# Performance work log

Hardware: AMD Instinct MI355X
Metric: run time of the kernel (lower is better)

Reference implementation:

```python
import jax, jax.numpy as jnp
import numpy as np

B, T, D = 4, 1024, 1024
N_HEAD, HEAD, LATENT = 16, 64, 32
N_EXP, TOP_K, N_FF = 8, 2, 4096
HID = int(2 * N_FF / 3)  # 2730, Expert hidden when ffn_multiplier is None
CAP_FACTOR = 1.0


def setup_inputs() -> dict:
    key = jax.random.key(0)
    ks = jax.random.split(key, 14)
    s = 0.02
    f = lambda k, shp: jax.random.normal(k, shp, jnp.float32) * s
    return dict(
        x=jax.random.normal(ks[0], (B, T, D), jnp.float32),
        noise_eps=jax.random.normal(ks[1], (B, T, N_EXP), jnp.float32),
        ln1_w=jnp.ones((D,), jnp.float32),
        ln2_w=jnp.ones((D,), jnp.float32),
        q_w=f(ks[2], (N_HEAD, D, HEAD)), q_b=jnp.zeros((N_HEAD, HEAD), jnp.float32),
        ka_w=f(ks[3], (N_HEAD, D, LATENT)), kb_w=f(ks[4], (N_HEAD, LATENT, HEAD)),
        va_w=f(ks[5], (N_HEAD, D, LATENT)), vb_w=f(ks[6], (N_HEAD, LATENT, HEAD)),
        proj_w=f(ks[7], (D, D)), proj_b=jnp.zeros((D,), jnp.float32),
        route_w=f(ks[8], (D, N_EXP)), route_b=jnp.zeros((N_EXP,), jnp.float32),
        noise_w=f(ks[9], (D, N_EXP)), noise_b=jnp.zeros((N_EXP,), jnp.float32),
        swiglu_w=f(ks[10], (N_EXP, D, 2 * HID)),
        down_w=f(ks[11], (N_EXP, HID, D)),
    )


def _rms(x, w, eps=1e-5):
    x32 = x.astype(jnp.float32)
    n = x32 * jax.lax.rsqrt(jnp.mean(x32 * x32, -1, keepdims=True) + eps)
    return n.astype(x.dtype) * w


def _rope(q, k):
    # q,k: [B,H,T,hd]; even/odd split then concatenated halves (matches torch code)
    hd, Tq = q.shape[-1], q.shape[-2]
    inv = 1.0 / (10000.0 ** (jnp.arange(0, hd, 2, dtype=jnp.float32) / hd))
    ang = jnp.arange(Tq, dtype=jnp.float32)[:, None] * inv[None, :]  # [T, hd/2]
    cos, sin = jnp.cos(ang), jnp.sin(ang)
    def rot(t):
        t1, t2 = t[..., ::2], t[..., 1::2]
        return jnp.concatenate([t1 * cos - t2 * sin, t1 * sin + t2 * cos], -1)
    return rot(q), rot(k)


def reference(x, noise_eps, ln1_w, ln2_w, q_w, q_b, ka_w, kb_w, va_w, vb_w,
              proj_w, proj_b, route_w, route_b, noise_w, noise_b, swiglu_w, down_w):
    Bx, Tx, Dm = x.shape
    hd = q_w.shape[-1]
    E = route_w.shape[-1]
    # ---- Multi-Head Latent Attention (pre-norm) ----
    xn = _rms(x, ln1_w)
    q = jnp.einsum('btd,hde->bhte', xn, q_w) + q_b[None, :, None, :]
    k = jnp.einsum('bhtl,hle->bhte', jnp.einsum('btd,hdl->bhtl', xn, ka_w), kb_w)
    v = jnp.einsum('bhtl,hle->bhte', jnp.einsum('btd,hdl->bhtl', xn, va_w), vb_w)
    q, k = _rope(q, k)
    scores = jnp.einsum('bhtd,bhsd->bhts', q, k) / jnp.sqrt(jnp.float32(hd))
    attn = jax.nn.softmax(scores, axis=-1)  # NOTE: no causal mask in source
    o = jnp.einsum('bhts,bhsd->bhtd', attn, v)
    o = o.transpose(0, 2, 1, 3).reshape(Bx, Tx, Dm)
    x = x + (o @ proj_w + proj_b)
    # ---- Noisy top-k router ----
    xn2 = _rms(x, ln2_w)
    logits = xn2 @ route_w + route_b
    noisy = logits + noise_eps * jax.nn.softplus(xn2 @ noise_w + noise_b)  # temperature=1
    _, topi = jax.lax.top_k(noisy, TOP_K)  # [B,T,k]
    sel = jnp.any(jax.nn.one_hot(topi, E, dtype=jnp.bool_), axis=-2)  # [B,T,E]
    probs = jax.nn.softmax(jnp.where(sel, noisy, -jnp.inf), axis=-1)
    aux = jnp.sum((jnp.mean(probs, (0, 1)) - 1.0 / E) ** 2)
    # ---- Capacity-limited expert dispatch (first-come in flat token order) ----
    N = Bx * Tx
    cap = int(N * TOP_K / E * CAP_FACTOR)
    flat_x = xn2.reshape(N, Dm)
    flat_p = probs.reshape(N, E)
    flat_i = topi.reshape(N, TOP_K)
    upd = jnp.zeros((N, Dm), x.dtype)
    for e in range(E):
        m = jnp.any(flat_i == e, axis=-1)            # [N]
        pos = jnp.cumsum(m) - 1                      # slot within expert buffer
        keep = m & (pos < cap)
        slot = jnp.where(keep, pos, cap)             # dropped -> overflow slot
        tok = jnp.zeros(cap + 1, jnp.int32).at[slot].set(jnp.arange(N, dtype=jnp.int32))[:cap]
        valid = jnp.zeros(cap + 1, jnp.bool_).at[slot].set(keep)[:cap]
        xe = flat_x[tok] * valid[:, None]            # [cap, D]; zero rows yield zero output (no biases)
        h = xe @ swiglu_w[e]
        h1, h2 = jnp.split(h, 2, axis=-1)
        oe = (jax.nn.silu(h1) * h2) @ down_w[e]
        gate = jnp.where(valid, flat_p[tok, e], 0.0)
        upd = upd.at[tok].add(oe * gate[:, None])
    return x + upd.reshape(Bx, Tx, Dm), aux
```

## Files before the change

### kernel.cpp

```cpp
#include <hip/hip_runtime.h>
#include <math.h>

#define NTOK   4096
#define DM     1024
#define NHEAD  16
#define HDIM   64
#define NEXP   8
#define CAP    1024
#define HID    2730
#define NFF2   5460
#define HIDP   2752

typedef __attribute__((ext_vector_type(8))) short bf16x8;
typedef __attribute__((ext_vector_type(4))) float f32x4;
typedef __attribute__((ext_vector_type(8))) _Float16 h16x8;
typedef __attribute__((ext_vector_type(4))) _Float16 h16x4;
typedef __attribute__((ext_vector_type(8))) unsigned short u16x8;

__device__ __forceinline__ unsigned short f2bf(float f) {
  unsigned int u = __float_as_uint(f);
  u += 0x7fffu + ((u >> 16) & 1u);
  return (unsigned short)(u >> 16);
}

__global__ void pack_kernel(const float* __restrict__ q_w, const float* __restrict__ ka_w,
                            const float* __restrict__ va_w, float* __restrict__ Wq,
                            float* __restrict__ Wlat) {
  int idx = blockIdx.x * 256 + threadIdx.x;
  if (idx < 1048576) {
    int d = idx >> 10, nn = idx & 1023;
    int h = nn >> 6, e = nn & 63;
    Wq[idx] = q_w[((size_t)h * 1024 + d) * 64 + e];
  } else {
    int j = idx - 1048576;
    int d = j >> 10, nn = j & 1023;
    if (nn < 512) {
      int h = nn >> 5, l = nn & 31;
      Wlat[j] = ka_w[((size_t)h * 1024 + d) * 32 + l];
    } else {
      int c = nn - 512;
      int h = c >> 5, l = c & 31;
      Wlat[j] = va_w[((size_t)h * 1024 + d) * 32 + l];
    }
  }
}

__global__ __launch_bounds__(256) void pack_swiglu(const float* __restrict__ swiglu_w,
                                                   unsigned short* __restrict__ Wpk) {
  int b = blockIdx.x;
  int kc32 = b & 31;
  int ejt = b >> 5;
  int jt = ejt % 43;
  int e = ejt / 43;
  int tid = threadIdx.x;
  int col = tid & 63;
  int k0 = (tid >> 6) * 8;
  int n = jt * 64 + col;
  bool nv = n < HID;
  const float* src = swiglu_w + ((size_t)e * DM + kc32 * 32 + k0) * NFF2 + n;
  u16x8 o1, o2;
#pragma unroll
  for (int j = 0; j < 8; j++) {
    float v1 = nv ? src[(size_t)j * NFF2] : 0.f;
    float v2 = nv ? src[(size_t)j * NFF2 + HID] : 0.f;
    o1[j] = f2bf(v1);
    o2[j] = f2bf(v2);
  }
  unsigned short* dst = Wpk + (size_t)b * 4096 + col * 32 + k0;
  *(u16x8*)dst = o1;
  *(u16x8*)(dst + 2048) = o2;
}

template <bool DUAL>
__global__ __launch_bounds__(256) void rms_kernel(const float* __restrict__ x,
                                                  const float* __restrict__ w,
                                                  float* __restrict__ out,
                                                  unsigned short* __restrict__ outb) {
  int row = blockIdx.x;
  int tid = threadIdx.x;
  const float4 v = ((const float4*)(x + (size_t)row * DM))[tid];
  float ss = v.x * v.x + v.y * v.y + v.z * v.z + v.w * v.w;
#pragma unroll
  for (int off = 32; off >= 1; off >>= 1) ss += __shfl_down(ss, off);
  __shared__ float red[4];
  if ((tid & 63) == 0) red[tid >> 6] = ss;
  __syncthreads();
  float tot = red[0] + red[1] + red[2] + red[3];
  float scale = rsqrtf(tot * (1.0f / 1024.0f) + 1e-5f);
  const float4 wv = ((const float4*)w)[tid];
  float4 o;
  o.x = v.x * scale * wv.x; o.y = v.y * scale * wv.y;
  o.z = v.z * scale * wv.z; o.w = v.w * scale * wv.w;
  ((float4*)(out + (size_t)row * DM))[tid] = o;
  if (DUAL) {
    ushort4 ob;
    ob.x = f2bf(o.x); ob.y = f2bf(o.y); ob.z = f2bf(o.z); ob.w = f2bf(o.w);
    *(ushort4*)(outb + (size_t)row * DM + tid * 4) = ob;
  }
}

template <bool BIAS, bool RES>
__global__ __launch_bounds__(256) void mfma_dense(const float* __restrict__ A,
                                                  const float* __restrict__ Bm,
                                                  const float* __restrict__ bias,
                                                  const float* __restrict__ res,
                                                  float* __restrict__ C, int K, int N) {
  int m0 = blockIdx.x * 128;
  int n0 = blockIdx.y * 128;
  __shared__ short As[128][40];
  __shared__ short Bs[128][40];
  int tid = threadIdx.x;
  int wid = tid >> 6, lane = tid & 63;
  int wm0 = (wid >> 1) * 64, wn0 = (wid & 1) * 64;
  int lr = lane & 15, lq = lane >> 4;
  f32x4 c[4][4];
  f32x4 zz = {0.f, 0.f, 0.f, 0.f};
#pragma unroll
  for (int i = 0; i < 4; i++)
#pragma unroll
    for (int j = 0; j < 4; j++) c[i][j] = zz;
  int ar = tid >> 2;
  int aq = tid & 3;
  int bn = tid & 127;
  int bh = tid >> 7;
  const float* Bp = Bm + n0 + bn;
  for (int kc = 0; kc < K; kc += 32) {
    __syncthreads();
#pragma unroll
    for (int rr = 0; rr < 2; rr++) {
      int row = rr * 64 + ar;
      const float* ap = A + (size_t)(m0 + row) * K + kc + aq * 8;
      float4 a0 = *(const float4*)ap;
      float4 a1 = *(const float4*)(ap + 4);
      u16x8 pk;
      pk[0] = f2bf(a0.x); pk[1] = f2bf(a0.y); pk[2] = f2bf(a0.z); pk[3] = f2bf(a0.w);
      pk[4] = f2bf(a1.x); pk[5] = f2bf(a1.y); pk[6] = f2bf(a1.z); pk[7] = f2bf(a1.w);
      *(u16x8*)&As[row][aq * 8] = pk;
    }
    {
      const float* bp = Bp + (size_t)(kc + bh * 16) * N;
      u16x8 p0, p1;
#pragma unroll
      for (int j = 0; j < 8; j++) p0[j] = f2bf(bp[(size_t)j * N]);
#pragma unroll
      for (int j = 0; j < 8; j++) p1[j] = f2bf(bp[(size_t)(j + 8) * N]);
      *(u16x8*)&Bs[bn][bh * 16] = p0;
      *(u16x8*)&Bs[bn][bh * 16 + 8] = p1;
    }
    __syncthreads();
    bf16x8 a[4], b[4];
#pragma unroll
    for (int mi = 0; mi < 4; mi++) a[mi] = *(bf16x8*)&As[wm0 + mi * 16 + lr][lq * 8];
#pragma unroll
    for (int ni = 0; ni < 4; ni++) b[ni] = *(bf16x8*)&Bs[wn0 + ni * 16 + lr][lq * 8];
#pragma unroll
    for (int mi = 0; mi < 4; mi++)
#pragma unroll
      for (int ni = 0; ni < 4; ni++)
        c[mi][ni] = __builtin_amdgcn_mfma_f32_16x16x32_bf16(a[mi], b[ni], c[mi][ni], 0, 0, 0);
  }
#pragma unroll
  for (int mi = 0; mi < 4; mi++)
#pragma unroll
    for (int ni = 0; ni < 4; ni++) {
      int nn = n0 + wn0 + ni * 16 + lr;
      float bv = BIAS ? bias[nn] : 0.f;
#pragma unroll
      for (int r = 0; r < 4; r++) {
        int mm = m0 + wm0 + mi * 16 + lq * 4 + r;
        float v = c[mi][ni][r] + bv;
        if (RES) v += res[(size_t)mm * N + nn];
        C[(size_t)mm * N + nn] = v;
      }
    }
}

__global__ void expand_kernel(const float* __restrict__ latents, const float* __restrict__ kb_w,
                              const float* __restrict__ vb_w, float* __restrict__ kpre,
                              _Float16* __restrict__ vf) {
  int idx = blockIdx.x * 256 + threadIdx.x;
  int e = idx & 63;
  int t = (idx >> 6) & 1023;
  int h = (idx >> 16) & 15;
  int b = idx >> 20;
  const float* lrow = latents + ((size_t)(b * 1024 + t)) * DM;
  const float* kb = kb_w + (size_t)h * 2048;
  const float* vb = vb_w + (size_t)h * 2048;
  float ka = 0.f, va = 0.f;
#pragma unroll
  for (int l = 0; l < 32; l++) {
    ka += lrow[h * 32 + l] * kb[l * 64 + e];
    va += lrow[512 + h * 32 + l] * vb[l * 64 + e];
  }
  kpre[idx] = ka;
  vf[idx] = (_Float16)va;
}

template <bool IN_BTHD>
__global__ void rope_kernel(const float* __restrict__ in, _Float16* __restrict__ out) {
  int idx = blockIdx.x * 256 + threadIdx.x;
  int i = idx & 31;
  int t = (idx >> 5) & 1023;
  int h = (idx >> 15) & 15;
  int b = idx >> 19;
  size_t ib;
  if (IN_BTHD)
    ib = ((size_t)(b * 1024 + t)) * DM + h * 64;
  else
    ib = ((size_t)((b * 16 + h) * 1024 + t)) * 64;
  float t1 = in[ib + 2 * i], t2 = in[ib + 2 * i + 1];
  float inv = exp2f(-(float)i * 0.41524101186091903f);
  float ang = (float)t * inv;
  float s, c;
  sincosf(ang, &s, &c);
  size_t ob = ((size_t)((b * 16 + h) * 1024 + t)) * 64;
  out[ob + i] = (_Float16)(t1 * c - t2 * s);
  out[ob + 32 + i] = (_Float16)(t1 * s + t2 * c);
}

__global__ __launch_bounds__(256) void attn_mfma(const _Float16* __restrict__ qf,
                                                 const _Float16* __restrict__ kf,
                                                 const _Float16* __restrict__ vf,
                                                 float* __restrict__ o) {
  __shared__ _Float16 Ks[64][72];
  __shared__ _Float16 Vt[64][68];
  int bh = blockIdx.y;
  int q0 = blockIdx.x * 64;
  int tid = threadIdx.x;
  int wv = tid >> 6, lane = tid & 63;
  int lr = lane & 15, lq = lane >> 4;
  const size_t base = (size_t)bh * 1024 * 64;
  const _Float16* qrow = qf + base + (size_t)(q0 + wv * 16 + lr) * 64;
  h16x8 qfr[2];
  qfr[0] = *(const h16x8*)(qrow + lq * 8);
  qfr[1] = *(const h16x8*)(qrow + 32 + lq * 8);
  float mrow = -3.0e38f, lsum = 0.f;
  f32x4 oacc[4];
  f32x4 zz = {0.f, 0.f, 0.f, 0.f};
#pragma unroll
  for (int i = 0; i < 4; i++) oacc[i] = zz;
  int skey = tid >> 2, spart = tid & 3;
  int vkey = tid & 63, vdb = (tid >> 6) * 16;

  for (int kt = 0; kt < 16; kt++) {
    __syncthreads();
    {
      const _Float16* kg = kf + base + (size_t)(kt * 64 + skey) * 64 + spart * 16;
      *(h16x8*)&Ks[skey][spart * 16] = *(const h16x8*)kg;
      *(h16x8*)&Ks[skey][spart * 16 + 8] = *(const h16x8*)(kg + 8);
      const _Float16* vg = vf + base + (size_t)(kt * 64 + vkey) * 64 + vdb;
      h16x8 v0 = *(const h16x8*)vg;
      h16x8 v1 = *(const h16x8*)(vg + 8);
#pragma unroll
      for (int j = 0; j < 8; j++) {
        Vt[vdb + j][vkey] = v0[j];
        Vt[vdb + 8 + j][vkey] = v1[j];
      }
    }
    __syncthreads();
    f32x4 st[4];
#pragma unroll
    for (int ni = 0; ni < 4; ni++) {
      st[ni] = zz;
#pragma unroll
      for (int kc = 0; kc < 2; kc++) {
        h16x8 ak = *(const h16x8*)&Ks[ni * 16 + lr][kc * 32 + lq * 8];
        st[ni] = __builtin_amdgcn_mfma_f32_16x16x32_f16(ak, qfr[kc], st[ni], 0, 0, 0);
      }
    }
    float smax = -3.0e38f;
#pragma unroll
    for (int ni = 0; ni < 4; ni++)
#pragma unroll
      for (int r = 0; r < 4; r++) {
        st[ni][r] *= 0.125f;
        smax = fmaxf(smax, st[ni][r]);
      }
    smax = fmaxf(smax, __shfl_xor(smax, 16));
    smax = fmaxf(smax, __shfl_xor(smax, 32));
    float newm = fmaxf(mrow, smax);
    float alpha = expf(mrow - newm);
    float rsum = 0.f;
    h16x4 pf[4];
#pragma unroll
    for (int ni = 0; ni < 4; ni++)
#pragma unroll
      for (int r = 0; r < 4; r++) {
        float p = expf(st[ni][r] - newm);
        rsum += p;
        pf[ni][r] = (_Float16)p;
      }
    rsum += __shfl_xor(rsum, 16);
    rsum += __shfl_xor(rsum, 32);
    lsum = lsum * alpha + rsum;
    mrow = newm;
#pragma unroll
    for (int dt = 0; dt < 4; dt++) {
      oacc[dt][0] *= alpha; oacc[dt][1] *= alpha;
      oacc[dt][2] *= alpha; oacc[dt][3] *= alpha;
    }
#pragma unroll
    for (int dt = 0; dt < 4; dt++)
#pragma unroll
      for (int ni = 0; ni < 4; ni++) {
        h16x4 va = *(const h16x4*)&Vt[dt * 16 + lr][ni * 16 + lq * 4];
        oacc[dt] = __builtin_amdgcn_mfma_f32_16x16x16f16(va, pf[ni], oacc[dt], 0, 0, 0);
      }
  }
  int b = bh >> 4, h = bh & 15;
  int qg = q0 + wv * 16 + lr;
  float invl = 1.0f / lsum;
  float* orow = o + (size_t)(b * 1024 + qg) * DM + h * 64;
#pragma unroll
  for (int dt = 0; dt < 4; dt++)
#pragma unroll
    for (int r = 0; r < 4; r++) orow[dt * 16 + lq * 4 + r] = oacc[dt][r] * invl;
}

__global__ __launch_bounds__(256) void router_kernel(
    const float* __restrict__ xn2, const float* __restrict__ route_w,
    const float* __restrict__ route_b, const float* __restrict__ noise_w,
    const float* __restrict__ noise_b, const float* __restrict__ noise_eps,
    int* __restrict__ topi, float* __restrict__ flat_p, float* __restrict__ probsum,
    int* __restrict__ slotmap) {
  int wave = threadIdx.x >> 6;
  int lane = threadIdx.x & 63;
  int tk = blockIdx.x * 4 + wave;
  float acc[8] = {0.f}, nacc[8] = {0.f};
  const float* xr = xn2 + (size_t)tk * DM;
  for (int it = 0; it < 16; it++) {
    int d = it * 64 + lane;
    float xv = xr[d];
    const float* rw = route_w + d * 8;
    const float* nw = noise_w + d * 8;
#pragma unroll
    for (int e = 0; e < 8; e++) {
      acc[e] += xv * rw[e];
      nacc[e] += xv * nw[e];
    }
  }
#pragma unroll
  for (int off = 32; off >= 1; off >>= 1) {
#pragma unroll
    for (int e = 0; e < 8; e++) {
      acc[e] += __shfl_down(acc[e], off);
      nacc[e] += __shfl_down(nacc[e], off);
    }
  }
  if (lane == 0) {
    float noisy[8];
#pragma unroll
    for (int e = 0; e < 8; e++) {
      float lg = acc[e] + route_b[e];
      float nl = nacc[e] + noise_b[e];
      float sp = (nl > 20.f) ? nl : log1pf(expf(nl));
      noisy[e] = lg + noise_eps[tk * 8 + e] * sp;
    }
    int i1 = 0;
    float n1 = noisy[0];
#pragma unroll
    for (int e = 1; e < 8; e++)
      if (noisy[e] > n1) { n1 = noisy[e]; i1 = e; }
    int i2 = -1;
    float n2 = -3.0e38f;
#pragma unroll
    for (int e = 0; e < 8; e++)
      if (e != i1 && noisy[e] > n2) { n2 = noisy[e]; i2 = e; }
    float r = expf(n2 - n1);
    float p1 = 1.0f / (1.0f + r);
    float p2 = r / (1.0f + r);
    topi[tk * 2] = i1;
    topi[tk * 2 + 1] = i2;
#pragma unroll
    for (int e = 0; e < 8; e++) flat_p[tk * 8 + e] = (e == i1) ? p1 : ((e == i2) ? p2 : 0.f);
    atomicAdd(&probsum[i1], p1);
    atomicAdd(&probsum[i2], p2);
    slotmap[tk * 2] = -1;
    slotmap[tk * 2 + 1] = -1;
  }
}

__global__ __launch_bounds__(512) void scan_kernel(const int* __restrict__ topi,
                                                   const float* __restrict__ flat_p,
                                                   int* __restrict__ tok, float* __restrict__ gate,
                                                   int* __restrict__ cnt, int* __restrict__ slotmap) {
  int e = threadIdx.x >> 6;
  int lane = threadIdx.x & 63;
  int count = 0;
  for (int base = 0; base < NTOK; base += 64) {
    int t = base + lane;
    int a = topi[t * 2], b = topi[t * 2 + 1];
    bool mflag = (a == e) || (b == e);
    unsigned long long mask = __ballot(mflag);
    int pos = count + __popcll(mask & ((1ull << lane) - 1ull));
    if (mflag && pos < CAP) {
      tok[e * CAP + pos] = t;
      gate[e * CAP + pos] = flat_p[t * 8 + e];
      int k = (a == e) ? 0 : 1;
      slotmap[t * 2 + k] = pos;
    }
    count += __popcll(mask);
  }
  if (lane == 0) cnt[e] = (count < CAP) ? count : CAP;
}

template <bool PACKED>
__global__ __launch_bounds__(256) void mfma_swiglu(const unsigned short* __restrict__ xn2b,
                                                   const float* __restrict__ swiglu_w,
                                                   const unsigned short* __restrict__ Wpk,
                                                   const int* __restrict__ tok,
                                                   const int* __restrict__ cnt,
                                                   unsigned short* __restrict__ ACT) {
  int L = blockIdx.x;
  int e = L & 7;
  int gw = L >> 3;
  int m0 = (gw & 7) * 128;
  int jt = gw >> 3;
  int j0 = jt * 64;
  __shared__ short As[128][40];
  __shared__ short B1s[64][40];
  __shared__ short B2s[64][40];
  __shared__ int tokL[128];
  int tid = threadIdx.x;
  if (tid < 128) {
    int slot = m0 + tid;
    tokL[tid] = (slot < cnt[e]) ? tok[e * CAP + slot] : -1;
  }
  __syncthreads();
  int wid = tid >> 6, lane = tid & 63;
  int wm0 = (wid >> 1) * 64, wn0 = (wid & 1) * 32;
  int lr = lane & 15, lq = lane >> 4;
  f32x4 c1[4][2], c2[4][2];
  f32x4 zz = {0.f, 0.f, 0.f, 0.f};
#pragma unroll
  for (int i = 0; i < 4; i++)
#pragma unroll
    for (int j = 0; j < 2; j++) { c1[i][j] = zz; c2[i][j] = zz; }
  int ar = tid >> 2;
  int aq = tid & 3;
  int tr0 = tokL[ar], tr1 = tokL[64 + ar];
  const unsigned short* wbase = Wpk + (size_t)(e * 43 + jt) * 32 * 4096;
  int bnn = tid & 63;
  int bkq = tid >> 6;
  int col = j0 + bnn;
  bool cvalid = col < HID;
  const float* Wb = swiglu_w + (size_t)e * DM * NFF2;
  const float* Wc1 = Wb + col;
  const float* Wc2 = Wb + HID + col;

  for (int kc = 0; kc < DM; kc += 32) {
    __syncthreads();
    {
      float4 av = {0.f, 0.f, 0.f, 0.f};
      if (tr0 >= 0) av = *(const float4*)(xn2b + (size_t)tr0 * DM + kc + aq * 8);
      *(float4*)&As[ar][aq * 8] = av;
      float4 av2 = {0.f, 0.f, 0.f, 0.f};
      if (tr1 >= 0) av2 = *(const float4*)(xn2b + (size_t)tr1 * DM + kc + aq * 8);
      *(float4*)&As[64 + ar][aq * 8] = av2;
    }
    if (PACKED) {
      const unsigned short* wp = wbase + (size_t)(kc >> 5) * 4096;
      u16x8 k1 = *(const u16x8*)(wp + tid * 8);
      u16x8 k2 = *(const u16x8*)(wp + 2048 + tid * 8);
      *(u16x8*)&B1s[tid >> 2][(tid & 3) * 8] = k1;
      *(u16x8*)&B2s[tid >> 2][(tid & 3) * 8] = k2;
    } else {
      const float* p1 = Wc1 + (size_t)(kc + bkq * 8) * NFF2;
      const float* p2 = Wc2 + (size_t)(kc + bkq * 8) * NFF2;
      u16x8 k1, k2;
#pragma unroll
      for (int j = 0; j < 8; j++) {
        float v1 = cvalid ? p1[(size_t)j * NFF2] : 0.f;
        float v2 = cvalid ? p2[(size_t)j * NFF2] : 0.f;
        k1[j] = f2bf(v1);
        k2[j] = f2bf(v2);
      }
      *(u16x8*)&B1s[bnn][bkq * 8] = k1;
      *(u16x8*)&B2s[bnn][bkq * 8] = k2;
    }
    __syncthreads();
    bf16x8 a[4], b1[2], b2[2];
#pragma unroll
    for (int mi = 0; mi < 4; mi++) a[mi] = *(bf16x8*)&As[wm0 + mi * 16 + lr][lq * 8];
#pragma unroll
    for (int ni = 0; ni < 2; ni++) {
      b1[ni] = *(bf16x8*)&B1s[wn0 + ni * 16 + lr][lq * 8];
      b2[ni] = *(bf16x8*)&B2s[wn0 + ni * 16 + lr][lq * 8];
    }
#pragma unroll
    for (int mi = 0; mi < 4; mi++)
#pragma unroll
      for (int ni = 0; ni < 2; ni++) {
        c1[mi][ni] = __builtin_amdgcn_mfma_f32_16x16x32_bf16(a[mi], b1[ni], c1[mi][ni], 0, 0, 0);
        c2[mi][ni] = __builtin_amdgcn_mfma_f32_16x16x32_bf16(a[mi], b2[ni], c2[mi][ni], 0, 0, 0);
      }
  }
#pragma unroll
  for (int mi = 0; mi < 4; mi++)
#pragma unroll
    for (int ni = 0; ni < 2; ni++)
#pragma unroll
      for (int r = 0; r < 4; r++) {
        int mm = m0 + wm0 + mi * 16 + lq * 4 + r;
        int cc = j0 + wn0 + ni * 16 + lr;
        float h1 = c1[mi][ni][r], h2 = c2[mi][ni][r];
        float act = (h1 / (1.0f + expf(-h1))) * h2;
        ACT[(size_t)e * CAP * HIDP + (size_t)mm * HIDP + cc] = f2bf(act);
      }
}

__global__ __launch_bounds__(256) void mfma_down(const unsigned short* __restrict__ ACT,
                                                 const float* __restrict__ down_w,
                                                 float* __restrict__ OE) {
  int L = blockIdx.x;
  int e = L & 7;
  int gw = L >> 3;
  int m0 = (gw & 7) * 128;
  int n0 = (gw >> 3) * 128;
  __shared__ short As[128][40];
  __shared__ short Bs[128][40];
  int tid = threadIdx.x;
  int wid = tid >> 6, lane = tid & 63;
  int wm0 = (wid >> 1) * 64, wn0 = (wid & 1) * 64;
  int lr = lane & 15, lq = lane >> 4;
  f32x4 c[4][4];
  f32x4 zz = {0.f, 0.f, 0.f, 0.f};
#pragma unroll
  for (int i = 0; i < 4; i++)
#pragma unroll
    for (int j = 0; j < 4; j++) c[i][j] = zz;
  const unsigned short* Ab = ACT + (size_t)e * CAP * HIDP + (size_t)m0 * HIDP;
  const float* Bb = down_w + (size_t)e * HID * DM + n0;
  int ar = tid >> 2;
  int aq = tid & 3;
  int bnn = tid & 127;
  int bh = tid >> 7;
  const float* Bp = Bb + bnn;

  for (int kc = 0; kc < HIDP; kc += 32) {
    __syncthreads();
    *(float4*)&As[ar][aq * 8] = *(const float4*)(Ab + (size_t)ar * HIDP + kc + aq * 8);
    *(float4*)&As[64 + ar][aq * 8] = *(const float4*)(Ab + (size_t)(64 + ar) * HIDP + kc + aq * 8);
    {
      int kb = kc + bh * 16;
      u16x8 p0, p1;
#pragma unroll
      for (int j = 0; j < 8; j++) {
        float v = (kb + j < HID) ? Bp[(size_t)(kb + j) * DM] : 0.f;
        p0[j] = f2bf(v);
      }
#pragma unroll
      for (int j = 0; j < 8; j++) {
        float v = (kb + 8 + j < HID) ? Bp[(size_t)(kb + 8 + j) * DM] : 0.f;
        p1[j] = f2bf(v);
      }
      *(u16x8*)&Bs[bnn][bh * 16] = p0;
      *(u16x8*)&Bs[bnn][bh * 16 + 8] = p1;
    }
    __syncthreads();
    bf16x8 a[4], b[4];
#pragma unroll
    for (int mi = 0; mi < 4; mi++) a[mi] = *(bf16x8*)&As[wm0 + mi * 16 + lr][lq * 8];
#pragma unroll
    for (int ni = 0; ni < 4; ni++) b[ni] = *(bf16x8*)&Bs[wn0 + ni * 16 + lr][lq * 8];
#pragma unroll
    for (int mi = 0; mi < 4; mi++)
#pragma unroll
      for (int ni = 0; ni < 4; ni++)
        c[mi][ni] = __builtin_amdgcn_mfma_f32_16x16x32_bf16(a[mi], b[ni], c[mi][ni], 0, 0, 0);
  }
#pragma unroll
  for (int mi = 0; mi < 4; mi++)
#pragma unroll
    for (int ni = 0; ni < 4; ni++)
#pragma unroll
      for (int r = 0; r < 4; r++) {
        int mm = m0 + wm0 + mi * 16 + lq * 4 + r;
        int nn = n0 + wn0 + ni * 16 + lr;
        OE[((size_t)e << 20) + (size_t)mm * DM + nn] = c[mi][ni][r];
      }
}

__global__ void combine_kernel(const float* __restrict__ x2, const float* __restrict__ OE,
                               const int* __restrict__ topi, const int* __restrict__ slotmap,
                               const float* __restrict__ flat_p, float* __restrict__ out) {
  int idx = blockIdx.x * 256 + threadIdx.x;
  int t = idx >> 8;
  int c4 = (idx & 255) * 4;
  float4 v = *(const float4*)(x2 + (size_t)t * DM + c4);
#pragma unroll
  for (int k = 0; k < 2; k++) {
    int s = slotmap[t * 2 + k];
    if (s >= 0) {
      int e = topi[t * 2 + k];
      float g = flat_p[t * 8 + e];
      float4 ov = *(const float4*)(OE + ((size_t)e << 20) + (size_t)s * DM + c4);
      v.x += g * ov.x; v.y += g * ov.y; v.z += g * ov.z; v.w += g * ov.w;
    }
  }
  *(float4*)(out + (size_t)t * DM + c4) = v;
}

__global__ void aux_kernel(const float* __restrict__ probsum, float* __restrict__ out) {
  if (threadIdx.x == 0) {
    float s = 0.f;
#pragma unroll
    for (int e = 0; e < 8; e++) {
      float d = probsum[e] * (1.0f / 4096.0f) - 0.125f;
      s += d * d;
    }
    out[4194304] = s;
  }
}

extern "C" void kernel_launch(void* const* d_in, const int* in_sizes, int n_in, void* d_out,
                              int out_size, void* d_ws, size_t ws_size, hipStream_t stream) {
  const float* x = (const float*)d_in[0];
  const float* noise_eps = (const float*)d_in[1];
  const float* ln1_w = (const float*)d_in[2];
  const float* ln2_w = (const float*)d_in[3];
  const float* q_w = (const float*)d_in[4];
  const float* q_b = (const float*)d_in[5];
  const float* ka_w = (const float*)d_in[6];
  const float* kb_w = (const float*)d_in[7];
  const float* va_w = (const float*)d_in[8];
  const float* vb_w = (const float*)d_in[9];
  const float* proj_w = (const float*)d_in[10];
  const float* proj_b = (const float*)d_in[11];
  const float* route_w = (const float*)d_in[12];
  const float* route_b = (const float*)d_in[13];
  const float* noise_w = (const float*)d_in[14];
  const float* noise_b = (const float*)d_in[15];
  const float* swiglu_w = (const float*)d_in[16];
  const float* down_w = (const float*)d_in[17];
  float* out = (float*)d_out;
  char* w = (char*)d_ws;
  const size_t MB = 1ull << 20;

  bool packed = ws_size >= (size_t)172 * MB;

  float* xn = (float*)(w + 0 * MB);
  float* qtmp = (float*)(w + 16 * MB);
  float* latents = (float*)(w + 32 * MB);
  float* kpre = (float*)(w + 48 * MB);
  _Float16* qfb = (_Float16*)(w + 64 * MB);
  _Float16* kfb = (_Float16*)(w + 72 * MB);
  _Float16* vfb = (_Float16*)(w + 80 * MB);
  float* ob = (float*)(w + 88 * MB);
  float* Wq = (float*)(w + 104 * MB);
  float* Wlat = (float*)(w + 108 * MB);
  float* x2 = (float*)(w + 44 * MB);
  float* xn2 = (float*)(w + 60 * MB);
  unsigned short* Wpk = (unsigned short*)(w + 76 * MB);
  unsigned short* ACT = (unsigned short*)(w + 0 * MB);
  float* OE = (float*)(w + 76 * MB);
  unsigned short* xn2b = (unsigned short*)(w + (packed ? 162 : 108) * MB);
  char* sm = w + (packed ? 170 : 116) * MB;
  int* topi = (int*)sm;
  int* tok = (int*)(sm + 64 * 1024);
  int* cntb = (int*)(sm + 128 * 1024);
  int* slotmap = (int*)(sm + 192 * 1024);
  float* flat_p = (float*)(sm + 256 * 1024);
  float* gateb = (float*)(sm + 512 * 1024);
  float* probsum = (float*)(sm + 576 * 1024);

  pack_kernel<<<8192, 256, 0, stream>>>(q_w, ka_w, va_w, Wq, Wlat);
  rms_kernel<false><<<4096, 256, 0, stream>>>(x, ln1_w, xn, nullptr);
  mfma_dense<true, false><<<dim3(32, 8), 256, 0, stream>>>(xn, Wq, q_b, nullptr, qtmp, 1024, 1024);
  mfma_dense<false, false><<<dim3(32, 8), 256, 0, stream>>>(xn, Wlat, nullptr, nullptr, latents, 1024, 1024);
  expand_kernel<<<16384, 256, 0, stream>>>(latents, kb_w, vb_w, kpre, vfb);
  rope_kernel<true><<<8192, 256, 0, stream>>>(qtmp, qfb);
  rope_kernel<false><<<8192, 256, 0, stream>>>(kpre, kfb);
  attn_mfma<<<dim3(16, 64), 256, 0, stream>>>(qfb, kfb, vfb, ob);
  mfma_dense<true, true><<<dim3(32, 8), 256, 0, stream>>>(ob, proj_w, proj_b, x, x2, 1024, 1024);
  if (packed) {
    pack_swiglu<<<11008, 256, 0, stream>>>(swiglu_w, Wpk);
  }
  rms_kernel<true><<<4096, 256, 0, stream>>>(x2, ln2_w, xn2, xn2b);
  hipMemsetAsync(probsum, 0, 8 * sizeof(float), stream);
  router_kernel<<<1024, 256, 0, stream>>>(xn2, route_w, route_b, noise_w, noise_b, noise_eps,
                                          topi, flat_p, probsum, slotmap);
  scan_kernel<<<1, 512, 0, stream>>>(topi, flat_p, tok, gateb, cntb, slotmap);
  if (packed) {
    mfma_swiglu<true><<<2752, 256, 0, stream>>>(xn2b, swiglu_w, Wpk, tok, cntb, ACT);
  } else {
    mfma_swiglu<false><<<2752, 256, 0, stream>>>(xn2b, swiglu_w, Wpk, tok, cntb, ACT);
  }
  mfma_down<<<512, 256, 0, stream>>>(ACT, down_w, OE);
  combine_kernel<<<4096, 256, 0, stream>>>(x2, OE, topi, slotmap, flat_p, out);
  aux_kernel<<<1, 64, 0, stream>>>(probsum, out);
}
```

Measured before the change: 1.086 ms.

## Pre-pack all GEMM weights to bf16 tiles and prefetch operands in registers

Adds packing kernels that convert the q/latent/proj and down-projection weights into bf16 k-tiled layouts, so the GEMM inner loops do coalesced vector loads instead of strided fp32 loads with per-element conversion. Activations feeding the dense GEMMs (RMS output, attention output) are now stored as bf16. All MFMA GEMMs gain a register prefetch of the next k-tile that overlaps global loads with compute. The workspace layout is reorganised and the unpacked fallback path is removed. In exchange, extra pack passes over down_w and proj_w are added every call, and the workspace must be large enough for the packed buffers.

```diff
diff --git a/kernel.cpp b/kernel.cpp
--- a/kernel.cpp
+++ b/kernel.cpp
@@ -10,6 +10,7 @@
 #define HID    2730
 #define NFF2   5460
 #define HIDP   2752
+#define KCD    86
 
 typedef __attribute__((ext_vector_type(8))) short bf16x8;
 typedef __attribute__((ext_vector_type(4))) float f32x4;
@@ -23,25 +24,43 @@
   return (unsigned short)(u >> 16);
 }
 
-__global__ void pack_kernel(const float* __restrict__ q_w, const float* __restrict__ ka_w,
-                            const float* __restrict__ va_w, float* __restrict__ Wq,
-                            float* __restrict__ Wlat) {
-  int idx = blockIdx.x * 256 + threadIdx.x;
-  if (idx < 1048576) {
-    int d = idx >> 10, nn = idx & 1023;
-    int h = nn >> 6, e = nn & 63;
-    Wq[idx] = q_w[((size_t)h * 1024 + d) * 64 + e];
+__global__ __launch_bounds__(256) void pack_dense3(const float* __restrict__ q_w,
+                                                   const float* __restrict__ ka_w,
+                                                   const float* __restrict__ va_w,
+                                                   const float* __restrict__ proj_w,
+                                                   unsigned short* __restrict__ Wqt,
+                                                   unsigned short* __restrict__ Wlatt,
+                                                   unsigned short* __restrict__ Wprojt) {
+  int b = blockIdx.x;
+  int tid = threadIdx.x;
+  int col = tid & 63;
+  int k0 = (tid >> 6) * 8;
+  int which = b >> 9;
+  int bb = b & 511;
+  int nt = bb >> 5, kc = bb & 31;
+  int d0 = kc * 32 + k0;
+  u16x8 o;
+  if (which == 0) {
+    const float* src = q_w + ((size_t)nt * 1024 + d0) * 64 + col;
+#pragma unroll
+    for (int j = 0; j < 8; j++) o[j] = f2bf(src[(size_t)j * 64]);
+    *(u16x8*)(Wqt + (size_t)bb * 2048 + col * 32 + k0) = o;
+  } else if (which == 1) {
+    int n = nt * 64 + col;
+    const float* base;
+    int h, l;
+    if (n < 512) { h = n >> 5; l = n & 31; base = ka_w; }
+    else { int m = n - 512; h = m >> 5; l = m & 31; base = va_w; }
+    const float* src = base + ((size_t)h * 1024 + d0) * 32 + l;
+#pragma unroll
+    for (int j = 0; j < 8; j++) o[j] = f2bf(src[(size_t)j * 32]);
+    *(u16x8*)(Wlatt + (size_t)bb * 2048 + col * 32 + k0) = o;
   } else {
-    int j = idx - 1048576;
-    int d = j >> 10, nn = j & 1023;
-    if (nn < 512) {
-      int h = nn >> 5, l = nn & 31;
-      Wlat[j] = ka_w[((size_t)h * 1024 + d) * 32 + l];
-    } else {
-      int c = nn - 512;
-      int h = c >> 5, l = c & 31;
-      Wlat[j] = va_w[((size_t)h * 1024 + d) * 32 + l];
-    }
+    int n = nt * 64 + col;
+    const float* src = proj_w + (size_t)d0 * 1024 + n;
+#pragma unroll
+    for (int j = 0; j < 8; j++) o[j] = f2bf(src[(size_t)j * 1024]);
+    *(u16x8*)(Wprojt + (size_t)bb * 2048 + col * 32 + k0) = o;
   }
 }
 
@@ -71,7 +90,28 @@
   *(u16x8*)(dst + 2048) = o2;
 }
 
-template <bool DUAL>
+__global__ __launch_bounds__(256) void pack_down(const float* __restrict__ down_w,
+                                                 unsigned short* __restrict__ Wdk) {
+  int b = blockIdx.x;
+  int kci = b % KCD;
+  int ent = b / KCD;
+  int nt = ent & 15;
+  int e = ent >> 4;
+  int tid = threadIdx.x;
+  int col = tid & 63, k0 = (tid >> 6) * 8;
+  int n = nt * 64 + col;
+  int kbase = kci * 32 + k0;
+  const float* src = down_w + ((size_t)e * HID + kbase) * DM + n;
+  u16x8 o;
+#pragma unroll
+  for (int j = 0; j < 8; j++) {
+    float v = (kbase + j < HID) ? src[(size_t)j * DM] : 0.f;
+    o[j] = f2bf(v);
+  }
+  *(u16x8*)(Wdk + (size_t)b * 2048 + col * 32 + k0) = o;
+}
+
+template <bool F32OUT>
 __global__ __launch_bounds__(256) void rms_kernel(const float* __restrict__ x,
                                                   const float* __restrict__ w,
                                                   float* __restrict__ out,
@@ -91,22 +131,21 @@
   float4 o;
   o.x = v.x * scale * wv.x; o.y = v.y * scale * wv.y;
   o.z = v.z * scale * wv.z; o.w = v.w * scale * wv.w;
-  ((float4*)(out + (size_t)row * DM))[tid] = o;
-  if (DUAL) {
-    ushort4 ob;
-    ob.x = f2bf(o.x); ob.y = f2bf(o.y); ob.z = f2bf(o.z); ob.w = f2bf(o.w);
-    *(ushort4*)(outb + (size_t)row * DM + tid * 4) = ob;
-  }
+  if (F32OUT) ((float4*)(out + (size_t)row * DM))[tid] = o;
+  ushort4 ob;
+  ob.x = f2bf(o.x); ob.y = f2bf(o.y); ob.z = f2bf(o.z); ob.w = f2bf(o.w);
+  *(ushort4*)(outb + (size_t)row * DM + tid * 4) = ob;
 }
 
 template <bool BIAS, bool RES>
-__global__ __launch_bounds__(256) void mfma_dense(const float* __restrict__ A,
-                                                  const float* __restrict__ Bm,
+__global__ __launch_bounds__(256) void mfma_dense(const unsigned short* __restrict__ A,
+                                                  const unsigned short* __restrict__ Bpk,
                                                   const float* __restrict__ bias,
                                                   const float* __restrict__ res,
                                                   float* __restrict__ C, int K, int N) {
   int m0 = blockIdx.x * 128;
   int n0 = blockIdx.y * 128;
+  int KC = K >> 5;
   __shared__ short As[128][40];
   __shared__ short Bs[128][40];
   int tid = threadIdx.x;
@@ -119,35 +158,27 @@
   for (int i = 0; i < 4; i++)
 #pragma unroll
     for (int j = 0; j < 4; j++) c[i][j] = zz;
-  int ar = tid >> 2;
-  int aq = tid & 3;
-  int bn = tid & 127;
-  int bh = tid >> 7;
-  const float* Bp = Bm + n0 + bn;
-  for (int kc = 0; kc < K; kc += 32) {
-    __syncthreads();
-#pragma unroll
-    for (int rr = 0; rr < 2; rr++) {
-      int row = rr * 64 + ar;
-      const float* ap = A + (size_t)(m0 + row) * K + kc + aq * 8;
-      float4 a0 = *(const float4*)ap;
-      float4 a1 = *(const float4*)(ap + 4);
-      u16x8 pk;
-      pk[0] = f2bf(a0.x); pk[1] = f2bf(a0.y); pk[2] = f2bf(a0.z); pk[3] = f2bf(a0.w);
-      pk[4] = f2bf(a1.x); pk[5] = f2bf(a1.y); pk[6] = f2bf(a1.z); pk[7] = f2bf(a1.w);
-      *(u16x8*)&As[row][aq * 8] = pk;
-    }
-    {
-      const float* bp = Bp + (size_t)(kc + bh * 16) * N;
-      u16x8 p0, p1;
-#pragma unroll
-      for (int j = 0; j < 8; j++) p0[j] = f2bf(bp[(size_t)j * N]);
-#pragma unroll
-      for (int j = 0; j < 8; j++) p1[j] = f2bf(bp[(size_t)(j + 8) * N]);
-      *(u16x8*)&Bs[bn][bh * 16] = p0;
-      *(u16x8*)&Bs[bn][bh * 16 + 8] = p1;
-    }
-    __syncthreads();
+  int ar = tid >> 2, aq = tid & 3;
+  const unsigned short* Ap0 = A + (size_t)(m0 + ar) * K + aq * 8;
+  const unsigned short* Ap1 = A + (size_t)(m0 + 64 + ar) * K + aq * 8;
+  const unsigned short* Bt = Bpk + (size_t)(n0 >> 6) * KC * 2048 + tid * 8;
+  u16x8 ra0 = *(const u16x8*)Ap0;
+  u16x8 ra1 = *(const u16x8*)Ap1;
+  u16x8 rb0 = *(const u16x8*)Bt;
+  u16x8 rb1 = *(const u16x8*)(Bt + (size_t)KC * 2048);
+  for (int kci = 0; kci < KC; kci++) {
+    __syncthreads();
+    *(u16x8*)&As[ar][aq * 8] = ra0;
+    *(u16x8*)&As[64 + ar][aq * 8] = ra1;
+    *(u16x8*)&Bs[tid >> 2][(tid & 3) * 8] = rb0;
+    *(u16x8*)&Bs[64 + (tid >> 2)][(tid & 3) * 8] = rb1;
+    __syncthreads();
+    if (kci + 1 < KC) {
+      ra0 = *(const u16x8*)(Ap0 + (kci + 1) * 32);
+      ra1 = *(const u16x8*)(Ap1 + (kci + 1) * 32);
+      rb0 = *(const u16x8*)(Bt + (size_t)(kci + 1) * 2048);
+      rb1 = *(const u16x8*)(Bt + (size_t)(KC + kci + 1) * 2048);
+    }
     bf16x8 a[4], b[4];
 #pragma unroll
     for (int mi = 0; mi < 4; mi++) a[mi] = *(bf16x8*)&As[wm0 + mi * 16 + lr][lq * 8];
@@ -221,7 +252,7 @@
 __global__ __launch_bounds__(256) void attn_mfma(const _Float16* __restrict__ qf,
                                                  const _Float16* __restrict__ kf,
                                                  const _Float16* __restrict__ vf,
-                                                 float* __restrict__ o) {
+                                                 unsigned short* __restrict__ o) {
   __shared__ _Float16 Ks[64][72];
   __shared__ _Float16 Vt[64][68];
   int bh = blockIdx.y;
@@ -310,11 +341,16 @@
   int b = bh >> 4, h = bh & 15;
   int qg = q0 + wv * 16 + lr;
   float invl = 1.0f / lsum;
-  float* orow = o + (size_t)(b * 1024 + qg) * DM + h * 64;
-#pragma unroll
-  for (int dt = 0; dt < 4; dt++)
-#pragma unroll
-    for (int r = 0; r < 4; r++) orow[dt * 16 + lq * 4 + r] = oacc[dt][r] * invl;
+  unsigned short* orow = o + (size_t)(b * 1024 + qg) * DM + h * 64;
+#pragma unroll
+  for (int dt = 0; dt < 4; dt++) {
+    ushort4 ov;
+    ov.x = f2bf(oacc[dt][0] * invl);
+    ov.y = f2bf(oacc[dt][1] * invl);
+    ov.z = f2bf(oacc[dt][2] * invl);
+    ov.w = f2bf(oacc[dt][3] * invl);
+    *(ushort4*)(orow + dt * 16 + lq * 4) = ov;
+  }
 }
 
 __global__ __launch_bounds__(256) void router_kernel(
@@ -404,9 +440,7 @@
   if (lane == 0) cnt[e] = (count < CAP) ? count : CAP;
 }
 
-template <bool PACKED>
 __global__ __launch_bounds__(256) void mfma_swiglu(const unsigned short* __restrict__ xn2b,
-                                                   const float* __restrict__ swiglu_w,
                                                    const unsigned short* __restrict__ Wpk,
                                                    const int* __restrict__ tok,
                                                    const int* __restrict__ cnt,
@@ -424,7 +458,7 @@
   int tid = threadIdx.x;
   if (tid < 128) {
     int slot = m0 + tid;
-    tokL[tid] = (slot < cnt[e]) ? tok[e * CAP + slot] : -1;
+    tokL[tid] = (slot < cnt[e]) ? tok[e * CAP + slot] : 0;
   }
   __syncthreads();
   int wid = tid >> 6, lane = tid & 63;
@@ -436,49 +470,28 @@
   for (int i = 0; i < 4; i++)
 #pragma unroll
     for (int j = 0; j < 2; j++) { c1[i][j] = zz; c2[i][j] = zz; }
-  int ar = tid >> 2;
-  int aq = tid & 3;
-  int tr0 = tokL[ar], tr1 = tokL[64 + ar];
-  const unsigned short* wbase = Wpk + (size_t)(e * 43 + jt) * 32 * 4096;
-  int bnn = tid & 63;
-  int bkq = tid >> 6;
-  int col = j0 + bnn;
-  bool cvalid = col < HID;
-  const float* Wb = swiglu_w + (size_t)e * DM * NFF2;
-  const float* Wc1 = Wb + col;
-  const float* Wc2 = Wb + HID + col;
-
-  for (int kc = 0; kc < DM; kc += 32) {
-    __syncthreads();
-    {
-      float4 av = {0.f, 0.f, 0.f, 0.f};
-      if (tr0 >= 0) av = *(const float4*)(xn2b + (size_t)tr0 * DM + kc + aq * 8);
-      *(float4*)&As[ar][aq * 8] = av;
-      float4 av2 = {0.f, 0.f, 0.f, 0.f};
-      if (tr1 >= 0) av2 = *(const float4*)(xn2b + (size_t)tr1 * DM + kc + aq * 8);
-      *(float4*)&As[64 + ar][aq * 8] = av2;
-    }
-    if (PACKED) {
-      const unsigned short* wp = wbase + (size_t)(kc >> 5) * 4096;
-      u16x8 k1 = *(const u16x8*)(wp + tid * 8);
-      u16x8 k2 = *(const u16x8*)(wp + 2048 + tid * 8);
-      *(u16x8*)&B1s[tid >> 2][(tid & 3) * 8] = k1;
-      *(u16x8*)&B2s[tid >> 2][(tid & 3) * 8] = k2;
-    } else {
-      const float* p1 = Wc1 + (size_t)(kc + bkq * 8) * NFF2;
-      const float* p2 = Wc2 + (size_t)(kc + bkq * 8) * NFF2;
-      u16x8 k1, k2;
-#pragma unroll
-      for (int j = 0; j < 8; j++) {
-        float v1 = cvalid ? p1[(size_t)j * NFF2] : 0.f;
-        float v2 = cvalid ? p2[(size_t)j * NFF2] : 0.f;
-        k1[j] = f2bf(v1);
-        k2[j] = f2bf(v2);
-      }
-      *(u16x8*)&B1s[bnn][bkq * 8] = k1;
-      *(u16x8*)&B2s[bnn][bkq * 8] = k2;
-    }
-    __syncthreads();
+  int ar = tid >> 2, aq = tid & 3;
+  const unsigned short* Ap0 = xn2b + (size_t)tokL[ar] * DM + aq * 8;
+  const unsigned short* Ap1 = xn2b + (size_t)tokL[64 + ar] * DM + aq * 8;
+  const unsigned short* wp = Wpk + (size_t)(e * 43 + jt) * 32 * 4096 + tid * 8;
+  u16x8 ra0 = *(const u16x8*)Ap0;
+  u16x8 ra1 = *(const u16x8*)Ap1;
+  u16x8 rb1 = *(const u16x8*)wp;
+  u16x8 rb2 = *(const u16x8*)(wp + 2048);
+
+  for (int kci = 0; kci < 32; kci++) {
+    __syncthreads();
+    *(u16x8*)&As[ar][aq * 8] = ra0;
+    *(u16x8*)&As[64 + ar][aq * 8] = ra1;
+    *(u16x8*)&B1s[tid >> 2][(tid & 3) * 8] = rb1;
+    *(u16x8*)&B2s[tid >> 2][(tid & 3) * 8] = rb2;
+    __syncthreads();
+    if (kci < 31) {
+      ra0 = *(const u16x8*)(Ap0 + (kci + 1) * 32);
+      ra1 = *(const u16x8*)(Ap1 + (kci + 1) * 32);
+      rb1 = *(const u16x8*)(wp + (size_t)(kci + 1) * 4096);
+      rb2 = *(const u16x8*)(wp + (size_t)(kci + 1) * 4096 + 2048);
+    }
     bf16x8 a[4], b1[2], b2[2];
 #pragma unroll
     for (int mi = 0; mi < 4; mi++) a[mi] = *(bf16x8*)&As[wm0 + mi * 16 + lr][lq * 8];
@@ -510,13 +523,14 @@
 }
 
 __global__ __launch_bounds__(256) void mfma_down(const unsigned short* __restrict__ ACT,
-                                                 const float* __restrict__ down_w,
+                                                 const unsigned short* __restrict__ Wdk,
                                                  float* __restrict__ OE) {
   int L = blockIdx.x;
   int e = L & 7;
   int gw = L >> 3;
   int m0 = (gw & 7) * 128;
-  int n0 = (gw >> 3) * 128;
+  int nt0 = (gw >> 3) * 2;
+  int n0 = nt0 * 64;
   __shared__ short As[128][40];
   __shared__ short Bs[128][40];
   int tid = threadIdx.x;
@@ -529,35 +543,29 @@
   for (int i = 0; i < 4; i++)
 #pragma unroll
     for (int j = 0; j < 4; j++) c[i][j] = zz;
+  int ar = tid >> 2, aq = tid & 3;
   const unsigned short* Ab = ACT + (size_t)e * CAP * HIDP + (size_t)m0 * HIDP;
-  const float* Bb = down_w + (size_t)e * HID * DM + n0;
-  int ar = tid >> 2;
-  int aq = tid & 3;
-  int bnn = tid & 127;
-  int bh = tid >> 7;
-  const float* Bp = Bb + bnn;
-
-  for (int kc = 0; kc < HIDP; kc += 32) {
-    __syncthreads();
-    *(float4*)&As[ar][aq * 8] = *(const float4*)(Ab + (size_t)ar * HIDP + kc + aq * 8);
-    *(float4*)&As[64 + ar][aq * 8] = *(const float4*)(Ab + (size_t)(64 + ar) * HIDP + kc + aq * 8);
-    {
-      int kb = kc + bh * 16;
-      u16x8 p0, p1;
-#pragma unroll
-      for (int j = 0; j < 8; j++) {
-        float v = (kb + j < HID) ? Bp[(size_t)(kb + j) * DM] : 0.f;
-        p0[j] = f2bf(v);
-      }
-#pragma unroll
-      for (int j = 0; j < 8; j++) {
-        float v = (kb + 8 + j < HID) ? Bp[(size_t)(kb + 8 + j) * DM] : 0.f;
-        p1[j] = f2bf(v);
-      }
-      *(u16x8*)&Bs[bnn][bh * 16] = p0;
-      *(u16x8*)&Bs[bnn][bh * 16 + 8] = p1;
-    }
-    __syncthreads();
+  const unsigned short* Ap0 = Ab + (size_t)ar * HIDP + aq * 8;
+  const unsigned short* Ap1 = Ab + (size_t)(64 + ar) * HIDP + aq * 8;
+  const unsigned short* Bt = Wdk + (size_t)(e * 16 + nt0) * KCD * 2048 + tid * 8;
+  u16x8 ra0 = *(const u16x8*)Ap0;
+  u16x8 ra1 = *(const u16x8*)Ap1;
+  u16x8 rb0 = *(const u16x8*)Bt;
+  u16x8 rb1 = *(const u16x8*)(Bt + (size_t)KCD * 2048);
+
+  for (int kci = 0; kci < KCD; kci++) {
+    __syncthreads();
+    *(u16x8*)&As[ar][aq * 8] = ra0;
+    *(u16x8*)&As[64 + ar][aq * 8] = ra1;
+    *(u16x8*)&Bs[tid >> 2][(tid & 3) * 8] = rb0;
+    *(u16x8*)&Bs[64 + (tid >> 2)][(tid & 3) * 8] = rb1;
+    __syncthreads();
+    if (kci + 1 < KCD) {
+      ra0 = *(const u16x8*)(Ap0 + (kci + 1) * 32);
+      ra1 = *(const u16x8*)(Ap1 + (kci + 1) * 32);
+      rb0 = *(const u16x8*)(Bt + (size_t)(kci + 1) * 2048);
+      rb1 = *(const u16x8*)(Bt + (size_t)(KCD + kci + 1) * 2048);
+    }
     bf16x8 a[4], b[4];
 #pragma unroll
     for (int mi = 0; mi < 4; mi++) a[mi] = *(bf16x8*)&As[wm0 + mi * 16 + lr][lq * 8];
@@ -637,25 +645,26 @@
   char* w = (char*)d_ws;
   const size_t MB = 1ull << 20;
 
-  bool packed = ws_size >= (size_t)172 * MB;
-
-  float* xn = (float*)(w + 0 * MB);
-  float* qtmp = (float*)(w + 16 * MB);
-  float* latents = (float*)(w + 32 * MB);
-  float* kpre = (float*)(w + 48 * MB);
-  _Float16* qfb = (_Float16*)(w + 64 * MB);
-  _Float16* kfb = (_Float16*)(w + 72 * MB);
-  _Float16* vfb = (_Float16*)(w + 80 * MB);
-  float* ob = (float*)(w + 88 * MB);
-  float* Wq = (float*)(w + 104 * MB);
-  float* Wlat = (float*)(w + 108 * MB);
-  float* x2 = (float*)(w + 44 * MB);
-  float* xn2 = (float*)(w + 60 * MB);
-  unsigned short* Wpk = (unsigned short*)(w + 76 * MB);
-  unsigned short* ACT = (unsigned short*)(w + 0 * MB);
-  float* OE = (float*)(w + 76 * MB);
-  unsigned short* xn2b = (unsigned short*)(w + (packed ? 162 : 108) * MB);
-  char* sm = w + (packed ? 170 : 116) * MB;
+  float* x2 = (float*)(w + 0 * MB);
+  float* xn2 = (float*)(w + 16 * MB);
+  unsigned short* xn2b = (unsigned short*)(w + 32 * MB);
+  char* sm = w + 40 * MB;
+  unsigned short* xnb = (unsigned short*)(w + 42 * MB);
+  float* qtmp = (float*)(w + 50 * MB);
+  float* latents = (float*)(w + 66 * MB);
+  float* kpre = (float*)(w + 82 * MB);
+  _Float16* qfb = (_Float16*)(w + 98 * MB);
+  _Float16* kfb = (_Float16*)(w + 106 * MB);
+  _Float16* vfb = (_Float16*)(w + 114 * MB);
+  unsigned short* obb = (unsigned short*)(w + 122 * MB);
+  unsigned short* Wqt = (unsigned short*)(w + 130 * MB);
+  unsigned short* Wlatt = (unsigned short*)(w + 132 * MB);
+  unsigned short* Wprojt = (unsigned short*)(w + 134 * MB);
+  unsigned short* Wpk = (unsigned short*)(w + 42 * MB);
+  unsigned short* ACT = (unsigned short*)(w + 128 * MB);
+  unsigned short* Wdk = (unsigned short*)(w + 42 * MB);
+  float* OE = (float*)(w + 86 * MB);
+
   int* topi = (int*)sm;
   int* tok = (int*)(sm + 64 * 1024);
   int* cntb = (int*)(sm + 128 * 1024);
@@ -664,29 +673,24 @@
   float* gateb = (float*)(sm + 512 * 1024);
   float* probsum = (float*)(sm + 576 * 1024);
 
-  pack_kernel<<<8192, 256, 0, stream>>>(q_w, ka_w, va_w, Wq, Wlat);
-  rms_kernel<false><<<4096, 256, 0, stream>>>(x, ln1_w, xn, nullptr);
-  mfma_dense<true, false><<<dim3(32, 8), 256, 0, stream>>>(xn, Wq, q_b, nullptr, qtmp, 1024, 1024);
-  mfma_dense<false, false><<<dim3(32, 8), 256, 0, stream>>>(xn, Wlat, nullptr, nullptr, latents, 1024, 1024);
+  pack_dense3<<<1536, 256, 0, stream>>>(q_w, ka_w, va_w, proj_w, Wqt, Wlatt, Wprojt);
+  rms_kernel<false><<<4096, 256, 0, stream>>>(x, ln1_w, nullptr, xnb);
+  mfma_dense<true, false><<<dim3(32, 8), 256, 0, stream>>>(xnb, Wqt, q_b, nullptr, qtmp, 1024, 1024);
+  mfma_dense<false, false><<<dim3(32, 8), 256, 0, stream>>>(xnb, Wlatt, nullptr, nullptr, latents, 1024, 1024);
   expand_kernel<<<16384, 256, 0, stream>>>(latents, kb_w, vb_w, kpre, vfb);
   rope_kernel<true><<<8192, 256, 0, stream>>>(qtmp, qfb);
   rope_kernel<false><<<8192, 256, 0, stream>>>(kpre, kfb);
-  attn_mfma<<<dim3(16, 64), 256, 0, stream>>>(qfb, kfb, vfb, ob);
-  mfma_dense<true, true><<<dim3(32, 8), 256, 0, stream>>>(ob, proj_w, proj_b, x, x2, 1024, 1024);
-  if (packed) {
-    pack_swiglu<<<11008, 256, 0, stream>>>(swiglu_w, Wpk);
-  }
+  attn_mfma<<<dim3(16, 64), 256, 0, stream>>>(qfb, kfb, vfb, obb);
+  mfma_dense<true, true><<<dim3(32, 8), 256, 0, stream>>>(obb, Wprojt, proj_b, x, x2, 1024, 1024);
+  pack_swiglu<<<11008, 256, 0, stream>>>(swiglu_w, Wpk);
   rms_kernel<true><<<4096, 256, 0, stream>>>(x2, ln2_w, xn2, xn2b);
   hipMemsetAsync(probsum, 0, 8 * sizeof(float), stream);
   router_kernel<<<1024, 256, 0, stream>>>(xn2, route_w, route_b, noise_w, noise_b, noise_eps,
                                           topi, flat_p, probsum, slotmap);
   scan_kernel<<<1, 512, 0, stream>>>(topi, flat_p, tok, gateb, cntb, slotmap);
-  if (packed) {
-    mfma_swiglu<true><<<2752, 256, 0, stream>>>(xn2b, swiglu_w, Wpk, tok, cntb, ACT);
-  } else {
-    mfma_swiglu<false><<<2752, 256, 0, stream>>>(xn2b, swiglu_w, Wpk, tok, cntb, ACT);
-  }
-  mfma_down<<<512, 256, 0, stream>>>(ACT, down_w, OE);
+  mfma_swiglu<<<2752, 256, 0, stream>>>(xn2b, Wpk, tok, cntb, ACT);
+  pack_down<<<11008, 256, 0, stream>>>(down_w, Wdk);
+  mfma_down<<<512, 256, 0, stream>>>(ACT, Wdk, OE);
   combine_kernel<<<4096, 256, 0, stream>>>(x2, OE, topi, slotmap, flat_p, out);
   aux_kernel<<<1, 64, 0, stream>>>(probsum, out);
 }
```

After: 942.3 us. -13.2%, faster.
